# Optimization experiments

Hardware: AMD Instinct MI355X
Metric: run time of the kernel (lower is better)

The kernel has to match this reference:

```python
import jax, jax.numpy as jnp
import numpy as np

D_MODEL = 1024
HEADS = 16
D_K = D_MODEL // HEADS
B, S = 4, 2048


def setup_inputs() -> dict:
    key = jax.random.key(0)
    ks = jax.random.split(key, 12)
    xav = float(np.sqrt(6.0 / (D_MODEL + D_MODEL)))  # xavier_uniform bound
    inp = {
        "query": jax.random.normal(ks[0], (B, S, D_MODEL), jnp.float32),
        "key": jax.random.normal(ks[1], (B, S, D_MODEL), jnp.float32),
        "value": jax.random.normal(ks[2], (B, S, D_MODEL), jnp.float32),
        # causal mask, broadcast over batch and heads: [1,1,S,S]
        "mask": jnp.tril(jnp.ones((S, S), jnp.int32))[None, None],
        "Wq": jax.random.uniform(ks[3], (D_MODEL, D_MODEL), jnp.float32, -xav, xav),
        "bq": jnp.zeros((D_MODEL,), jnp.float32),
        "Wk": jax.random.uniform(ks[4], (D_MODEL, D_MODEL), jnp.float32, -xav, xav),
        "bk": jnp.zeros((D_MODEL,), jnp.float32),
        "Wv": jax.random.uniform(ks[5], (D_MODEL, D_MODEL), jnp.float32, -xav, xav),
        "bv": jnp.zeros((D_MODEL,), jnp.float32),
        "Wo": jax.random.uniform(ks[6], (D_MODEL, D_MODEL), jnp.float32, -xav, xav),
        "bo": jnp.zeros((D_MODEL,), jnp.float32),
    }
    return inp


def reference(query, key, value, mask, Wq, bq, Wk, bk, Wv, bv, Wo, bo):
    b, s, d = query.shape
    # torch Linear: y = x @ W.T + b, W is [out, in]
    Q = (jnp.einsum("bsd,ed->bse", query, Wq) + bq).reshape(b, s, HEADS, D_K).transpose(0, 2, 1, 3)
    K = (jnp.einsum("bsd,ed->bse", key, Wk) + bk).reshape(b, -1, HEADS, D_K).transpose(0, 2, 1, 3)
    V = (jnp.einsum("bsd,ed->bse", value, Wv) + bv).reshape(b, -1, HEADS, D_K).transpose(0, 2, 1, 3)
    scale = 1.0 / jnp.sqrt(jnp.asarray(D_K, query.dtype))
    scores = jnp.einsum("bhqd,bhkd->bhqk", Q, K) * scale  # [B,H,S,S]
    scores = jnp.where(mask == 0, -jnp.inf, scores)
    attn = jax.nn.softmax(scores, axis=-1)
    attn = jnp.where(jnp.isnan(attn), jnp.zeros_like(attn), attn)  # nan-fix as in source
    out = jnp.einsum("bhqk,bhkd->bhqd", attn, V)
    out = out.transpose(0, 2, 1, 3).reshape(b, s, d)
    return jnp.einsum("bsd,ed->bse", out, Wo) + bo
```

## Files before the change

### kernel.cpp

```cpp
#include <hip/hip_runtime.h>
#include <hip/hip_bf16.h>

#define DM 1024
#define NHEADS 16
#define DKH 64
#define BATCH 4
#define SEQ 2048
#define MROWS (BATCH*SEQ)

typedef __attribute__((ext_vector_type(8))) short bf16x8;
typedef __attribute__((ext_vector_type(4))) short bf16x4;
typedef __attribute__((ext_vector_type(4))) float f32x4;
typedef __attribute__((ext_vector_type(16))) float f32x16;

#if __has_builtin(__builtin_amdgcn_exp2f)
#define EXP2(x) __builtin_amdgcn_exp2f(x)
#else
#define EXP2(x) exp2f(x)
#endif

__device__ __forceinline__ unsigned short f2bf(float f){
  unsigned u = __float_as_uint(f);
  u += 0x7fffu + ((u >> 16) & 1u);
  return (unsigned short)(u >> 16);
}

__device__ __forceinline__ unsigned pk2bf(float lo, float hi){
  union { __hip_bfloat162 h; unsigned u; } c;
  c.h = __float22bfloat162_rn(make_float2(lo, hi));
  return c.u;
}

__device__ __forceinline__ bf16x8 cvtA8(float4 a, float4 b){
  union { unsigned u[4]; bf16x8 v; } r;
  r.u[0] = pk2bf(a.x, a.y);
  r.u[1] = pk2bf(a.z, a.w);
  r.u[2] = pk2bf(b.x, b.y);
  r.u[3] = pk2bf(b.z, b.w);
  return r.v;
}

__device__ __forceinline__ void gload16(const unsigned short* g, unsigned short* l){
  __builtin_amdgcn_global_load_lds((const __attribute__((address_space(1))) void*)g,
                                   (__attribute__((address_space(3))) void*)l, 16, 0, 0);
}

struct ConvArgs { const float* src[4]; unsigned short* dst[4]; };

__global__ __launch_bounds__(256) void conv_w(ConvArgs a){
  const int t = blockIdx.x >> 10;
  const int boff = blockIdx.x & 1023;
  const float* __restrict__ src = a.src[t];
  unsigned short* __restrict__ dst = a.dst[t];
  const int i = (boff * 256 + threadIdx.x) * 4;
  const float4 v = *reinterpret_cast<const float4*>(src + i);
  ushort4 o;
  o.x = f2bf(v.x); o.y = f2bf(v.y); o.z = f2bf(v.z); o.w = f2bf(v.w);
  *reinterpret_cast<ushort4*>(dst + i) = o;
}

template<int MODE, int AFP32>
__global__ __launch_bounds__(256)
void gemm_bt(const void* __restrict__ Av, const unsigned short* __restrict__ Bw,
             const float* __restrict__ bias, void* __restrict__ out, float scale)
{
  const int K = 1024;
  __shared__ short a_sh[128*64];
  __shared__ short b_sh[128*64];
  const int tid  = threadIdx.x;
  const int lane = tid & 63;
  const int wid  = tid >> 6;
  const int wm = wid >> 1, wn = wid & 1;
  const int lin = blockIdx.x;
  const int xcd = lin & 7;
  const int i9  = lin >> 3;
  const int tileM = (8*xcd + (i9 >> 3)) * 128;
  const int tileN = (i9 & 7) * 128;

  f32x4 acc[4][4];
  #pragma unroll
  for (int i = 0; i < 4; i++)
    #pragma unroll
    for (int j = 0; j < 4; j++)
      acc[i][j] = (f32x4){0.f,0.f,0.f,0.f};

  const int lr = lane & 15;
  const int lg = lane >> 4;
  const int r8 = lane >> 3, c8 = lane & 7;
  const int srow = 8*wid + r8;
  const int sgrp = (c8 ^ r8) * 8;

  for (int k0 = 0; k0 < K; k0 += 64){
    bf16x8 ra[4];
    if constexpr (AFP32){
      const float* Af = (const float*)Av;
      #pragma unroll
      for (int i = 0; i < 4; i++){
        int v   = tid + 256*i;
        int row = v >> 3;
        int cg  = v & 7;
        const float4 f0 = *reinterpret_cast<const float4*>(Af + (size_t)(tileM+row)*K + k0 + cg*8);
        const float4 f1 = *reinterpret_cast<const float4*>(Af + (size_t)(tileM+row)*K + k0 + cg*8 + 4);
        ra[i] = cvtA8(f0, f1);
      }
    }
    __syncthreads();
    #pragma unroll
    for (int j = 0; j < 4; j++){
      gload16(Bw + (size_t)(tileN + srow + 32*j)*K + k0 + sgrp,
              (unsigned short*)&b_sh[(8*wid + 32*j)*64]);
    }
    if constexpr (AFP32){
      #pragma unroll
      for (int i = 0; i < 4; i++){
        int v   = tid + 256*i;
        int row = v >> 3;
        int cg  = v & 7;
        *reinterpret_cast<bf16x8*>(&a_sh[row*64 + ((cg ^ (row & 7)) * 8)]) = ra[i];
      }
    } else {
      const unsigned short* Ab = (const unsigned short*)Av;
      #pragma unroll
      for (int j = 0; j < 4; j++){
        gload16(Ab + (size_t)(tileM + srow + 32*j)*K + k0 + sgrp,
                (unsigned short*)&a_sh[(8*wid + 32*j)*64]);
      }
    }
    __syncthreads();

    #pragma unroll
    for (int kk = 0; kk < 64; kk += 32){
      bf16x8 af[4], bfr[4];
      const int g0 = lg + (kk >> 3);
      #pragma unroll
      for (int fm = 0; fm < 4; fm++){
        int row = wm*64 + fm*16 + lr;
        af[fm] = *reinterpret_cast<const bf16x8*>(&a_sh[row*64 + ((g0 ^ (row & 7)) * 8)]);
      }
      #pragma unroll
      for (int fn = 0; fn < 4; fn++){
        int row = wn*64 + fn*16 + lr;
        bfr[fn] = *reinterpret_cast<const bf16x8*>(&b_sh[row*64 + ((g0 ^ (row & 7)) * 8)]);
      }
      #pragma unroll
      for (int fm = 0; fm < 4; fm++)
        #pragma unroll
        for (int fn = 0; fn < 4; fn++)
          acc[fm][fn] = __builtin_amdgcn_mfma_f32_16x16x32_bf16(af[fm], bfr[fn], acc[fm][fn], 0, 0, 0);
    }
  }

  #pragma unroll
  for (int fm = 0; fm < 4; fm++){
    #pragma unroll
    for (int fn = 0; fn < 4; fn++){
      #pragma unroll
      for (int r = 0; r < 4; r++){
        int m = tileM + wm*64 + fm*16 + lg*4 + r;
        int n = tileN + wn*64 + fn*16 + lr;
        float val = acc[fm][fn][r] + bias[n];
        if (MODE == 0){
          val *= scale;
          int b = m >> 11, s = m & 2047, h = n >> 6, d = n & 63;
          ((unsigned short*)out)[(((size_t)(b*NHEADS + h)*SEQ + s)*DKH + d)] = f2bf(val);
        } else if (MODE == 1){
          int b = m >> 11, s = m & 2047, h = n >> 6, d = n & 63;
          ((unsigned short*)out)[(((size_t)(b*NHEADS + h)*DKH + d)*SEQ + s)] = f2bf(val);
        } else {
          ((float*)out)[(size_t)m*DM + n] = val;
        }
      }
    }
  }
}

__global__ __launch_bounds__(512, 2)
void attn_kernel(const unsigned short* __restrict__ Q, const unsigned short* __restrict__ Kb,
                 const unsigned short* __restrict__ Vt, unsigned short* __restrict__ Oout)
{
  __shared__ unsigned short k_sh[2][128*64];
  __shared__ unsigned short v_sh[2][64*128];
  const int lane = threadIdx.x & 63;
  const int w    = threadIdx.x >> 6;
  const int q32  = lane & 31;
  const int hi   = lane >> 5;
  const int l7   = lane & 7;
  const int bh = blockIdx.x;
  const int y  = (int)blockIdx.y;
  const int hiT = 15 - y;
  const int myTile = (w < 4) ? hiT : y;
  const int qb0 = myTile * 128;
  const int qw0 = qb0 + (w & 3) * 32;
  const int qglob = qw0 + q32;
  const int b = bh >> 4, h = bh & 15;
  const size_t kbase = (size_t)bh * SEQ * DKH;
  const size_t vbase = (size_t)bh * DKH * SEQ;

  const int r8 = lane >> 3, c8 = lane & 7;
  const size_t offK0 = (size_t)(16*w + r8)*DKH     + (size_t)((c8 ^ r8) * 8);
  const size_t offK1 = (size_t)(16*w + 8 + r8)*DKH + (size_t)((c8 ^ r8) * 8);
  const int ldsK0 = (16*w)*64, ldsK1 = (16*w + 8)*64;
  const int r4 = lane >> 4, c16 = lane & 15;
  const size_t offV0 = (size_t)(8*w + r4)*SEQ     + (size_t)((c16 ^ r4) * 8);
  const size_t offV1 = (size_t)(8*w + 4 + r4)*SEQ + (size_t)((c16 ^ (4 + r4)) * 8);
  const int ldsV0 = (8*w)*128, ldsV1 = (8*w + 4)*128;

  bf16x8 qf[4];
  #pragma unroll
  for (int dblk = 0; dblk < 4; dblk++){
    qf[dblk] = *reinterpret_cast<const bf16x8*>(Q + kbase + (size_t)qglob*DKH + dblk*16 + hi*8);
  }

  float mrun = -__builtin_inff();
  float llocal = 0.f;
  f32x16 o0, o1;
  #pragma unroll
  for (int r = 0; r < 16; r++){ o0[r] = 0.f; o1[r] = 0.f; }
  f32x16 zero16;
  #pragma unroll
  for (int r = 0; r < 16; r++) zero16[r] = 0.f;

  const int nkb = hiT + 1;

#define STAGE(kb_, bf_) do { \
    gload16(Kb + kbase + (size_t)(kb_)*8192 + offK0, (unsigned short*)&k_sh[bf_][ldsK0]); \
    gload16(Kb + kbase + (size_t)(kb_)*8192 + offK1, (unsigned short*)&k_sh[bf_][ldsK1]); \
    gload16(Vt + vbase + (size_t)(kb_)*128  + offV0, (unsigned short*)&v_sh[bf_][ldsV0]); \
    gload16(Vt + vbase + (size_t)(kb_)*128  + offV1, (unsigned short*)&v_sh[bf_][ldsV1]); \
  } while(0)

  STAGE(0, 0);
  __syncthreads();

  for (int kb = 0; kb < nkb; kb++){
    const int buf = kb & 1;
    if (kb + 1 < nkb) STAGE(kb + 1, buf ^ 1);

    const unsigned short* ks = k_sh[buf];
    const unsigned short* vs = v_sh[buf];

    #pragma unroll
    for (int c = 0; c < 4; c++){
      const int base_k = kb*128 + c*32;
      if (base_k <= qw0 + 31){
        f32x16 st;
        __builtin_amdgcn_s_setprio(1);
        {
          bf16x8 kf0 = *reinterpret_cast<const bf16x8*>(&ks[(c*32 + q32)*64 + (((0*2 + hi) ^ l7) * 8)]);
          st = __builtin_amdgcn_mfma_f32_32x32x16_bf16(kf0, qf[0], zero16, 0, 0, 0);
        }
        #pragma unroll
        for (int dblk = 1; dblk < 4; dblk++){
          bf16x8 kf = *reinterpret_cast<const bf16x8*>(&ks[(c*32 + q32)*64 + (((dblk*2 + hi) ^ l7) * 8)]);
          st = __builtin_amdgcn_mfma_f32_32x32x16_bf16(kf, qf[dblk], st, 0, 0, 0);
        }
        __builtin_amdgcn_s_setprio(0);

        if (base_k + 31 > qw0){
          #pragma unroll
          for (int r = 0; r < 16; r++){
            int kg = base_k + (r & 3) + 8*(r >> 2) + 4*hi;
            if (kg > qglob) st[r] = -__builtin_inff();
          }
        }

        float mt = st[0];
        #pragma unroll
        for (int r = 1; r < 16; r++) mt = fmaxf(mt, st[r]);
        mt = fmaxf(mt, __shfl_xor(mt, 32));

        if (__any(mt > mrun + 8.f)){
          const float mnew = fmaxf(mrun, mt);
          const float corr = EXP2(mrun - mnew);
          mrun = mnew;
          #pragma unroll
          for (int r = 0; r < 16; r++){ o0[r] *= corr; o1[r] *= corr; }
          llocal *= corr;
        }

        float p[16];
        #pragma unroll
        for (int r = 0; r < 16; r++) p[r] = EXP2(st[r] - mrun);
        {
          float s0 = (p[0]+p[1]) + (p[2]+p[3]);
          float s1 = (p[4]+p[5]) + (p[6]+p[7]);
          float s2 = (p[8]+p[9]) + (p[10]+p[11]);
          float s3 = (p[12]+p[13]) + (p[14]+p[15]);
          llocal += (s0+s1) + (s2+s3);
        }
        unsigned pkA0 = pk2bf(p[0],  p[1]),  pkA1 = pk2bf(p[2],  p[3]);
        unsigned pkB0 = pk2bf(p[4],  p[5]),  pkB1 = pk2bf(p[6],  p[7]);
        unsigned pkC0 = pk2bf(p[8],  p[9]),  pkC1 = pk2bf(p[10], p[11]);
        unsigned pkD0 = pk2bf(p[12], p[13]), pkD1 = pk2bf(p[14], p[15]);
        unsigned xA0 = __shfl_xor(pkA0, 32), xA1 = __shfl_xor(pkA1, 32);
        unsigned xB0 = __shfl_xor(pkB0, 32), xB1 = __shfl_xor(pkB1, 32);
        unsigned xC0 = __shfl_xor(pkC0, 32), xC1 = __shfl_xor(pkC1, 32);
        unsigned xD0 = __shfl_xor(pkD0, 32), xD1 = __shfl_xor(pkD1, 32);
        const bool lo = (hi == 0);
        union { unsigned u[4]; bf16x8 v; } f0, f1;
        f0.u[0] = lo ? pkA0 : xB0;
        f0.u[1] = lo ? pkA1 : xB1;
        f0.u[2] = lo ? xA0  : pkB0;
        f0.u[3] = lo ? xA1  : pkB1;
        f1.u[0] = lo ? pkC0 : xD0;
        f1.u[1] = lo ? pkC1 : xD1;
        f1.u[2] = lo ? xC0  : pkD0;
        f1.u[3] = lo ? xC1  : pkD1;

        __builtin_amdgcn_s_setprio(1);
        #pragma unroll
        for (int k16 = 0; k16 < 2; k16++){
          bf16x8 fr = k16 ? f1.v : f0.v;
          {
            bf16x8 vf = *reinterpret_cast<const bf16x8*>(
                &vs[(0*32 + q32)*128 + (((c*4 + k16*2 + hi) ^ l7) * 8)]);
            o0 = __builtin_amdgcn_mfma_f32_32x32x16_bf16(vf, fr, o0, 0, 0, 0);
          }
          {
            bf16x8 vf = *reinterpret_cast<const bf16x8*>(
                &vs[(1*32 + q32)*128 + (((c*4 + k16*2 + hi) ^ l7) * 8)]);
            o1 = __builtin_amdgcn_mfma_f32_32x32x16_bf16(vf, fr, o1, 0, 0, 0);
          }
        }
        __builtin_amdgcn_s_setprio(0);
      }
    }
    __syncthreads();
  }
#undef STAGE

  const float l = llocal + __shfl_xor(llocal, 32);
  const float inv = 1.0f / l;
  size_t ob = ((size_t)(b*SEQ + qglob))*DM + h*DKH;
  #pragma unroll
  for (int g = 0; g < 4; g++){
    ushort4 pk;
    pk.x = f2bf(o0[4*g+0]*inv); pk.y = f2bf(o0[4*g+1]*inv);
    pk.z = f2bf(o0[4*g+2]*inv); pk.w = f2bf(o0[4*g+3]*inv);
    *reinterpret_cast<ushort4*>(&Oout[ob + 8*g + 4*hi]) = pk;
    ushort4 pk2;
    pk2.x = f2bf(o1[4*g+0]*inv); pk2.y = f2bf(o1[4*g+1]*inv);
    pk2.z = f2bf(o1[4*g+2]*inv); pk2.w = f2bf(o1[4*g+3]*inv);
    *reinterpret_cast<ushort4*>(&Oout[ob + 32 + 8*g + 4*hi]) = pk2;
  }
}

extern "C" void kernel_launch(void* const* d_in, const int* in_sizes, int n_in,
                              void* d_out, int out_size, void* d_ws, size_t ws_size,
                              hipStream_t stream) {
  const float* query = (const float*)d_in[0];
  const float* key   = (const float*)d_in[1];
  const float* value = (const float*)d_in[2];
  const float* Wq = (const float*)d_in[4];
  const float* bq = (const float*)d_in[5];
  const float* Wk = (const float*)d_in[6];
  const float* bk = (const float*)d_in[7];
  const float* Wv = (const float*)d_in[8];
  const float* bv = (const float*)d_in[9];
  const float* Wo = (const float*)d_in[10];
  const float* bo = (const float*)d_in[11];
  float* out = (float*)d_out;

  char* ws = (char*)d_ws;
  const size_t SZ_X = (size_t)MROWS * DM * 2;
  const size_t SZ_W = (size_t)DM * DM * 2;
  unsigned short* wqb = (unsigned short*)(ws + 0);
  unsigned short* wkb = (unsigned short*)(ws + SZ_W);
  unsigned short* wvb = (unsigned short*)(ws + 2*SZ_W);
  unsigned short* wob = (unsigned short*)(ws + 3*SZ_W);
  unsigned short* Qb   = (unsigned short*)(ws + 4*SZ_W);
  unsigned short* Kbuf = (unsigned short*)(ws + 4*SZ_W + SZ_X);
  unsigned short* Vt   = (unsigned short*)(ws + 4*SZ_W + 2*SZ_X);
  unsigned short* attO = (unsigned short*)(ws + 4*SZ_W + 3*SZ_X);

  ConvArgs ca;
  ca.src[0] = Wq; ca.src[1] = Wk; ca.src[2] = Wv; ca.src[3] = Wo;
  ca.dst[0] = wqb; ca.dst[1] = wkb; ca.dst[2] = wvb; ca.dst[3] = wob;
  conv_w<<<4096, 256, 0, stream>>>(ca);

  const int NBLK = (MROWS/128) * (DM/128);
  const float qscale = 0.125f * 1.4426950408889634f;
  gemm_bt<1,1><<<NBLK, 256, 0, stream>>>(value, wvb, bv, (void*)Vt,   1.0f);
  gemm_bt<0,1><<<NBLK, 256, 0, stream>>>(query, wqb, bq, (void*)Qb,   qscale);
  gemm_bt<0,1><<<NBLK, 256, 0, stream>>>(key,   wkb, bk, (void*)Kbuf, 1.0f);

  attn_kernel<<<dim3(64, 8), 512, 0, stream>>>(Qb, Kbuf, Vt, attO);

  gemm_bt<2,0><<<NBLK, 256, 0, stream>>>(attO, wob, bo, (void*)out, 1.0f);
}
```

Before: 188.5 us.

## Split KV range across two wave groups per query tile with LDS merge

Before, each block paired a high and a low query tile across its two groups of four waves. Now each block owns a single 128-row query tile, and the two wave groups split each 128-key stage between them (two 32-key chunks each). At the end, the partial softmax states (m, l, O) are merged through shared memory. The grid doubles to 1024 blocks, which adds parallelism, but the pairing-based causal load balancing is lost and the merge adds epilogue cost.

```diff
diff --git a/kernel.cpp b/kernel.cpp
--- a/kernel.cpp
+++ b/kernel.cpp
@@ -185,12 +185,12 @@
   const int q32  = lane & 31;
   const int hi   = lane >> 5;
   const int l7   = lane & 7;
+  const int grpk = w >> 2;
+  const int wq   = w & 3;
   const int bh = blockIdx.x;
-  const int y  = (int)blockIdx.y;
-  const int hiT = 15 - y;
-  const int myTile = (w < 4) ? hiT : y;
-  const int qb0 = myTile * 128;
-  const int qw0 = qb0 + (w & 3) * 32;
+  const int qtile = 15 - (int)blockIdx.y;
+  const int qb0 = qtile * 128;
+  const int qw0 = qb0 + wq * 32;
   const int qglob = qw0 + q32;
   const int b = bh >> 4, h = bh & 15;
   const size_t kbase = (size_t)bh * SEQ * DKH;
@@ -220,7 +220,7 @@
   #pragma unroll
   for (int r = 0; r < 16; r++) zero16[r] = 0.f;
 
-  const int nkb = hiT + 1;
+  const int nse = qtile + 1;
 
 #define STAGE(kb_, bf_) do { \
     gload16(Kb + kbase + (size_t)(kb_)*8192 + offK0, (unsigned short*)&k_sh[bf_][ldsK0]); \
@@ -232,16 +232,17 @@
   STAGE(0, 0);
   __syncthreads();
 
-  for (int kb = 0; kb < nkb; kb++){
-    const int buf = kb & 1;
-    if (kb + 1 < nkb) STAGE(kb + 1, buf ^ 1);
+  for (int s = 0; s < nse; s++){
+    const int buf = s & 1;
+    if (s + 1 < nse) STAGE(s + 1, buf ^ 1);
 
     const unsigned short* ks = k_sh[buf];
     const unsigned short* vs = v_sh[buf];
 
     #pragma unroll
-    for (int c = 0; c < 4; c++){
-      const int base_k = kb*128 + c*32;
+    for (int ci = 0; ci < 2; ci++){
+      const int c = grpk*2 + ci;
+      const int base_k = s*128 + c*32;
       if (base_k <= qw0 + 31){
         f32x16 st;
         __builtin_amdgcn_s_setprio(1);
@@ -329,19 +330,45 @@
   }
 #undef STAGE
 
-  const float l = llocal + __shfl_xor(llocal, 32);
-  const float inv = 1.0f / l;
-  size_t ob = ((size_t)(b*SEQ + qglob))*DM + h*DKH;
-  #pragma unroll
-  for (int g = 0; g < 4; g++){
-    ushort4 pk;
-    pk.x = f2bf(o0[4*g+0]*inv); pk.y = f2bf(o0[4*g+1]*inv);
-    pk.z = f2bf(o0[4*g+2]*inv); pk.w = f2bf(o0[4*g+3]*inv);
-    *reinterpret_cast<ushort4*>(&Oout[ob + 8*g + 4*hi]) = pk;
-    ushort4 pk2;
-    pk2.x = f2bf(o1[4*g+0]*inv); pk2.y = f2bf(o1[4*g+1]*inv);
-    pk2.z = f2bf(o1[4*g+2]*inv); pk2.w = f2bf(o1[4*g+3]*inv);
-    *reinterpret_cast<ushort4*>(&Oout[ob + 32 + 8*g + 4*hi]) = pk2;
+  const float lrow = llocal + __shfl_xor(llocal, 32);
+  float* osh  = (float*)k_sh;
+  float* mlsh = (float*)v_sh;
+
+  if (w >= 4){
+    const int pw = w - 4;
+    #pragma unroll
+    for (int r = 0; r < 16; r++){
+      osh[r*256 + pw*64 + lane]        = o0[r];
+      osh[(16 + r)*256 + pw*64 + lane] = o1[r];
+    }
+    mlsh[0*256 + pw*64 + lane] = mrun;
+    mlsh[1*256 + pw*64 + lane] = lrow;
+  }
+  __syncthreads();
+  if (w < 4){
+    const float m1 = mlsh[0*256 + w*64 + lane];
+    const float l1 = mlsh[1*256 + w*64 + lane];
+    const float m  = fmaxf(mrun, m1);
+    const float c0 = EXP2(mrun - m);
+    const float c1 = EXP2(m1 - m);
+    const float l  = lrow*c0 + l1*c1;
+    const float inv = 1.0f / l;
+    size_t ob = ((size_t)(b*SEQ + qglob))*DM + h*DKH;
+    #pragma unroll
+    for (int g = 0; g < 4; g++){
+      ushort4 pk;
+      pk.x = f2bf((o0[4*g+0]*c0 + osh[(4*g+0)*256 + w*64 + lane]*c1)*inv);
+      pk.y = f2bf((o0[4*g+1]*c0 + osh[(4*g+1)*256 + w*64 + lane]*c1)*inv);
+      pk.z = f2bf((o0[4*g+2]*c0 + osh[(4*g+2)*256 + w*64 + lane]*c1)*inv);
+      pk.w = f2bf((o0[4*g+3]*c0 + osh[(4*g+3)*256 + w*64 + lane]*c1)*inv);
+      *reinterpret_cast<ushort4*>(&Oout[ob + 8*g + 4*hi]) = pk;
+      ushort4 pk2;
+      pk2.x = f2bf((o1[4*g+0]*c0 + osh[(16+4*g+0)*256 + w*64 + lane]*c1)*inv);
+      pk2.y = f2bf((o1[4*g+1]*c0 + osh[(16+4*g+1)*256 + w*64 + lane]*c1)*inv);
+      pk2.z = f2bf((o1[4*g+2]*c0 + osh[(16+4*g+2)*256 + w*64 + lane]*c1)*inv);
+      pk2.w = f2bf((o1[4*g+3]*c0 + osh[(16+4*g+3)*256 + w*64 + lane]*c1)*inv);
+      *reinterpret_cast<ushort4*>(&Oout[ob + 32 + 8*g + 4*hi]) = pk2;
+    }
   }
 }
 
@@ -384,7 +411,7 @@
   gemm_bt<0,1><<<NBLK, 256, 0, stream>>>(query, wqb, bq, (void*)Qb,   qscale);
   gemm_bt<0,1><<<NBLK, 256, 0, stream>>>(key,   wkb, bk, (void*)Kbuf, 1.0f);
 
-  attn_kernel<<<dim3(64, 8), 512, 0, stream>>>(Qb, Kbuf, Vt, attO);
+  attn_kernel<<<dim3(64, 16), 512, 0, stream>>>(Qb, Kbuf, Vt, attO);
 
   gemm_bt<2,0><<<NBLK, 256, 0, stream>>>(attO, wob, bo, (void*)out, 1.0f);
 }
```

Result: slower. 200.4 us (+6.3%).
